# Kernel optimization log

Hardware: AMD Instinct MI355X
Metric: run time of the kernel (lower is better)

## Reference

```python
import jax, jax.numpy as jnp
import numpy as np

N_EMBD = 1024
N_HEAD = 16
HEAD_DIM = N_EMBD // N_HEAD


def setup_inputs() -> dict:
    key = jax.random.key(0)
    k1, k2, k3 = jax.random.split(key, 3)
    x = jax.random.normal(k1, (2, 2048, N_EMBD), dtype=jnp.float32)
    # torch Linear weight shapes: c_attn [3*n_embd, n_embd], c_proj [n_embd, n_embd]
    w_attn = jax.random.normal(k2, (3 * N_EMBD, N_EMBD), dtype=jnp.float32) * 0.02
    w_proj = jax.random.normal(k3, (N_EMBD, N_EMBD), dtype=jnp.float32) * 0.02
    return {"x": x, "w_attn": w_attn, "w_proj": w_proj}


def reference(x, w_attn, w_proj):
    B, T, C = x.shape
    qkv = x @ w_attn.T  # [B,T,3C]
    q, k, v = jnp.split(qkv, 3, axis=2)
    # [B,T,H,D] -> [B,H,T,D]
    def heads(t):
        return t.reshape(B, T, N_HEAD, HEAD_DIM).transpose(0, 2, 1, 3)
    q, k, v = heads(q), heads(k), heads(v)
    scale = 1.0 / jnp.sqrt(jnp.asarray(HEAD_DIM, dtype=x.dtype))
    att = jnp.einsum('bhqd,bhkd->bhqk', q, k) * scale
    causal = jnp.tril(jnp.ones((T, T), dtype=bool))
    att = jnp.where(causal[None, None], att, jnp.asarray(-jnp.inf, dtype=att.dtype))
    att = jax.nn.softmax(att, axis=-1)
    y = jnp.einsum('bhqk,bhkd->bhqd', att, v)
    y = y.transpose(0, 2, 1, 3).reshape(B, T, C)
    return y @ w_proj.T
```

## Files before the change

### kernel.cpp

```cpp
#include <hip/hip_runtime.h>

#define BSZ 2
#define SEQ 2048
#define NEMBD 1024
#define NHEAD 16
#define HDIM 64
#define BT (BSZ * SEQ)
#define QKV_LD (3 * NEMBD)
#define SCALE_LOG2E 0.1803368665f

typedef unsigned short u16;
typedef __attribute__((ext_vector_type(8))) short short8;
typedef __attribute__((ext_vector_type(4))) float floatx4;
typedef __attribute__((ext_vector_type(4))) unsigned short ushort4v;

#define MFMA16(a, b, c) __builtin_amdgcn_mfma_f32_16x16x32_bf16(a, b, c, 0, 0, 0)

__device__ __forceinline__ void gload_lds16(const void* g, void* l) {
  __builtin_amdgcn_global_load_lds(
      (const __attribute__((address_space(1))) unsigned int*)(g),
      (__attribute__((address_space(3))) unsigned int*)(l), 16, 0, 0);
}

__device__ __forceinline__ u16 f2bf(float f) {
  unsigned int u = __builtin_bit_cast(unsigned int, f);
  u += 0x7FFFu + ((u >> 16) & 1u);
  return (u16)(u >> 16);
}

__device__ __forceinline__ float bf2f(u16 v) {
  return __builtin_bit_cast(float, (unsigned)v << 16);
}

#define N_X  (BT * NEMBD)
#define N_WA (QKV_LD * NEMBD)
#define N_WP (NEMBD * NEMBD)
__global__ __launch_bounds__(256) void cvt_all(const float* __restrict__ x,
                                               const float* __restrict__ wa,
                                               const float* __restrict__ wp,
                                               u16* __restrict__ xb,
                                               u16* __restrict__ wab,
                                               u16* __restrict__ wpb) {
  int i = (blockIdx.x * 256 + threadIdx.x) * 8;
  const float* src;
  u16* dst;
  if (i < N_X)            { src = x + i;              dst = xb + i; }
  else if (i < N_X + N_WA){ src = wa + (i - N_X);     dst = wab + (i - N_X); }
  else                    { src = wp + (i - N_X - N_WA); dst = wpb + (i - N_X - N_WA); }
  float4 a = *(const float4*)(src);
  float4 b = *(const float4*)(src + 4);
  short8 o;
  o[0] = (short)f2bf(a.x); o[1] = (short)f2bf(a.y);
  o[2] = (short)f2bf(a.z); o[3] = (short)f2bf(a.w);
  o[4] = (short)f2bf(b.x); o[5] = (short)f2bf(b.y);
  o[6] = (short)f2bf(b.z); o[7] = (short)f2bf(b.w);
  *(short8*)(dst) = o;
}

__global__ __launch_bounds__(256) void gemm_qkv(const u16* __restrict__ A,
                                                const u16* __restrict__ B,
                                                u16* __restrict__ qkb,
                                                u16* __restrict__ vtg) {
  __shared__ __align__(16) u16 As[128 * 64];
  __shared__ __align__(16) u16 Bs[128 * 64];
  const int t = threadIdx.x;
  const int lane = t & 63, w = t >> 6;
  const int l15 = lane & 15, quad = lane >> 4;
  const int wm = w >> 1, wn = w & 1;
  const int m0 = blockIdx.y * 128, n0 = blockIdx.x * 128;
  const int is_v = (n0 >= 2 * NEMBD);

  floatx4 acc[4][4] = {};

  for (int k0 = 0; k0 < NEMBD; k0 += 64) {
    __syncthreads();
#pragma unroll
    for (int is = 0; is < 4; ++is) {
      int s = is * 256 + t;
      int row = s >> 3, pos = s & 7;
      int kc = pos ^ (row & 7);
      gload_lds16(A + (size_t)(m0 + row) * NEMBD + k0 + kc * 8, &As[s * 8]);
      gload_lds16(B + (size_t)(n0 + row) * NEMBD + k0 + kc * 8, &Bs[s * 8]);
    }
    __syncthreads();
#pragma unroll
    for (int kh = 0; kh < 2; ++kh) {
      short8 af[4], bfr[4];
#pragma unroll
      for (int mt = 0; mt < 4; ++mt) {
        int row = wm * 64 + mt * 16 + l15;
        af[mt] = *(const short8*)&As[row * 64 + (((kh * 4 + quad) ^ (row & 7)) * 8)];
      }
#pragma unroll
      for (int nt = 0; nt < 4; ++nt) {
        int row = wn * 64 + nt * 16 + l15;
        bfr[nt] = *(const short8*)&Bs[row * 64 + (((kh * 4 + quad) ^ (row & 7)) * 8)];
      }
      if (is_v) {
#pragma unroll
        for (int mt = 0; mt < 4; ++mt)
#pragma unroll
          for (int nt = 0; nt < 4; ++nt)
            acc[mt][nt] = MFMA16(af[mt], bfr[nt], acc[mt][nt]);
      } else {
#pragma unroll
        for (int mt = 0; mt < 4; ++mt)
#pragma unroll
          for (int nt = 0; nt < 4; ++nt)
            acc[mt][nt] = MFMA16(bfr[nt], af[mt], acc[mt][nt]);
      }
    }
  }

  if (is_v) {
#pragma unroll
    for (int mt = 0; mt < 4; ++mt)
#pragma unroll
      for (int nt = 0; nt < 4; ++nt) {
        int hd = n0 + wn * 64 + nt * 16 + l15 - 2 * NEMBD;
        int token = m0 + wm * 64 + mt * 16 + quad * 4;
        int b = token >> 11, tp = token & (SEQ - 1);
        ushort4v pk;
#pragma unroll
        for (int r = 0; r < 4; ++r) pk[r] = f2bf(acc[mt][nt][r]);
        *(ushort4v*)&vtg[((size_t)(b * NEMBD + hd)) * SEQ + tp] = pk;
      }
  } else {
#pragma unroll
    for (int mt = 0; mt < 4; ++mt) {
      size_t token = (size_t)(m0 + wm * 64 + mt * 16 + l15);
#pragma unroll
      for (int nt = 0; nt < 4; ++nt) {
        int nc = n0 + wn * 64 + nt * 16 + quad * 4;
        ushort4v pk;
#pragma unroll
        for (int r = 0; r < 4; ++r) pk[r] = f2bf(acc[mt][nt][r]);
        *(ushort4v*)&qkb[token * 2048 + nc] = pk;
      }
    }
  }
}

__global__ __launch_bounds__(256) void attn_mfma4(const u16* __restrict__ qkb,
                                                  const u16* __restrict__ vtg,
                                                  u16* __restrict__ opart,
                                                  float* __restrict__ lpart) {
  const int bx = blockIdx.x;
  const int qt = 15 - (bx >> 6);
  const int r6 = bx & 63;
  const int bh = r6 >> 1, half = r6 & 1;
  const int b = bh >> 4, h = bh & 15;
  const int t = threadIdx.x, lane = t & 63, w = t >> 6;
  const int l15 = lane & 15, quad = lane >> 4;

  __shared__ __align__(16) u16 S[25600];
  u16* Qs  = S;
  u16* KV0 = S + 8192;
  u16* KV1 = S;
  u16* Pa  = S + 16384;

  const int kt0 = half ? (qt + 1) : 0;
  const int nkt = qt + 1;

  {
    const u16* qb = qkb + ((size_t)(b * SEQ + qt * 128)) * 2048 + h * HDIM;
#pragma unroll
    for (int is = 0; is < 4; ++is) {
      int s = is * 256 + t;
      int row = s >> 3, pos = s & 7;
      int kc = pos ^ (row & 7);
      gload_lds16(qb + (size_t)row * 2048 + kc * 8, &Qs[s * 8]);
    }
  }

#define STAGE_KV(KT, BUF)                                                      \
  {                                                                            \
    const u16* kb_ = qkb + ((size_t)(b * SEQ + (KT) * 64)) * 2048 + NEMBD + h * HDIM; \
    const u16* vb_ = vtg + ((size_t)(bh * 64)) * SEQ + (KT) * 64;              \
    _Pragma("unroll")                                                          \
    for (int is = 0; is < 2; ++is) {                                           \
      int s = is * 256 + t;                                                    \
      int row = s >> 3, pos = s & 7;                                           \
      int kc = pos ^ (row & 7);                                                \
      gload_lds16(kb_ + (size_t)row * 2048 + kc * 8, &(BUF)[s * 8]);           \
      gload_lds16(vb_ + (size_t)row * SEQ + kc * 8, &(BUF)[4096 + s * 8]);     \
    }                                                                          \
  }

  STAGE_KV(kt0, KV0);
  __syncthreads();

  short8 qf[2][2];
#pragma unroll
  for (int qs = 0; qs < 2; ++qs) {
    int qrow = w * 32 + qs * 16 + l15;
#pragma unroll
    for (int hf = 0; hf < 2; ++hf)
      qf[qs][hf] = *(const short8*)&Qs[qrow * 64 + (((hf * 4 + quad) ^ (qrow & 7)) * 8)];
  }
  __syncthreads();

  float rs[2] = {0.f, 0.f};
  floatx4 o_acc[2][4] = {};

#define COMPUTE_TILE(BUF, KT, MASKED)                                          \
  {                                                                            \
    floatx4 sacc[2][4];                                                        \
    _Pragma("unroll")                                                          \
    for (int nt = 0; nt < 4; ++nt) {                                           \
      int krow = nt * 16 + l15;                                                \
      short8 kf0 = *(const short8*)&(BUF)[krow * 64 + ((quad ^ (krow & 7)) * 8)]; \
      short8 kf1 = *(const short8*)&(BUF)[krow * 64 + (((4 + quad) ^ (krow & 7)) * 8)]; \
      _Pragma("unroll")                                                        \
      for (int qs = 0; qs < 2; ++qs) {                                         \
        floatx4 z = {0.f, 0.f, 0.f, 0.f};                                      \
        z = MFMA16(kf0, qf[qs][0], z);                                         \
        z = MFMA16(kf1, qf[qs][1], z);                                         \
        sacc[qs][nt] = z;                                                      \
      }                                                                        \
    }                                                                          \
    _Pragma("unroll")                                                          \
    for (int qs = 0; qs < 2; ++qs) {                                           \
      const int qg = qt * 128 + w * 32 + qs * 16 + l15;                        \
      const int kb0 = (KT) * 64 + quad * 4;                                    \
      _Pragma("unroll")                                                        \
      for (int nt = 0; nt < 4; ++nt) {                                         \
        ushort4v pk;                                                           \
        _Pragma("unroll")                                                      \
        for (int r = 0; r < 4; ++r) {                                          \
          float p = exp2f(fmaf(sacc[qs][nt][r], SCALE_LOG2E, -8.0f));          \
          if (MASKED && (kb0 + nt * 16 + r) > qg) p = 0.0f;                    \
          rs[qs] += p;                                                         \
          pk[r] = f2bf(p);                                                     \
        }                                                                      \
        *(ushort4v*)&Pa[(w * 32 + qs * 16 + l15) * 72 + nt * 16 + quad * 4] = pk; \
      }                                                                        \
    }                                                                          \
    short8 pf[2][2];                                                           \
    _Pragma("unroll")                                                          \
    for (int qs = 0; qs < 2; ++qs) {                                           \
      const int prow = w * 32 + qs * 16 + l15;                                 \
      pf[qs][0] = *(const short8*)&Pa[prow * 72 + quad * 8];                   \
      pf[qs][1] = *(const short8*)&Pa[prow * 72 + 32 + quad * 8];              \
    }                                                                          \
    _Pragma("unroll")                                                          \
    for (int nt = 0; nt < 4; ++nt) {                                           \
      int drow = nt * 16 + l15;                                                \
      short8 vf0 = *(const short8*)&(BUF)[4096 + drow * 64 + ((quad ^ (drow & 7)) * 8)]; \
      short8 vf1 = *(const short8*)&(BUF)[4096 + drow * 64 + (((4 + quad) ^ (drow & 7)) * 8)]; \
      _Pragma("unroll")                                                        \
      for (int qs = 0; qs < 2; ++qs) {                                         \
        o_acc[qs][nt] = MFMA16(pf[qs][0], vf0, o_acc[qs][nt]);                 \
        o_acc[qs][nt] = MFMA16(pf[qs][1], vf1, o_acc[qs][nt]);                 \
      }                                                                        \
    }                                                                          \
  }

  for (int i = 0; i < nkt; ++i) {
    const int kt = kt0 + i;
    u16* cur = (i & 1) ? KV1 : KV0;
    u16* nxt = (i & 1) ? KV0 : KV1;
    if (i + 1 < nkt) STAGE_KV(kt0 + i + 1, nxt);
    if (kt >= 2 * qt) { COMPUTE_TILE(cur, kt, 1); }
    else              { COMPUTE_TILE(cur, kt, 0); }
    __syncthreads();
  }
#undef COMPUTE_TILE
#undef STAGE_KV

#pragma unroll
  for (int qs = 0; qs < 2; ++qs) {
    rs[qs] += __shfl_xor(rs[qs], 16, 64);
    rs[qs] += __shfl_xor(rs[qs], 32, 64);
    if (quad == 0)
      lpart[((size_t)half * 32 + bh) * SEQ + qt * 128 + w * 32 + qs * 16 + l15] = rs[qs];
  }
  u16* ob = opart + (size_t)half * BT * NEMBD;
#pragma unroll
  for (int qs = 0; qs < 2; ++qs)
#pragma unroll
    for (int nt = 0; nt < 4; ++nt)
#pragma unroll
      for (int r = 0; r < 4; ++r) {
        size_t tok = (size_t)(b * SEQ + qt * 128 + w * 32 + qs * 16 + quad * 4 + r);
        ob[tok * NEMBD + h * HDIM + nt * 16 + l15] = f2bf(o_acc[qs][nt][r]);
      }
}

__global__ __launch_bounds__(256) void combine(const u16* __restrict__ opart,
                                               const float* __restrict__ lpart,
                                               u16* __restrict__ yb) {
  int idx = (blockIdx.x * 256 + threadIdx.x) * 4;
  int tok = idx >> 10, c = idx & 1023;
  int b = tok >> 11, q = tok & (SEQ - 1), h = c >> 6;
  float l = lpart[(size_t)(b * 16 + h) * SEQ + q] +
            lpart[(size_t)(32 + b * 16 + h) * SEQ + q];
  float inv = 1.0f / l;
  ushort4v o0 = *(const ushort4v*)&opart[idx];
  ushort4v o1 = *(const ushort4v*)&opart[(size_t)BT * NEMBD + idx];
  ushort4v yo;
#pragma unroll
  for (int j = 0; j < 4; ++j) {
    float f0 = bf2f(o0[j]);
    float f1 = bf2f(o1[j]);
    yo[j] = f2bf((f0 + f1) * inv);
  }
  *(ushort4v*)&yb[idx] = yo;
}

__global__ __launch_bounds__(256) void gemm_out(const u16* __restrict__ A,
                                                const u16* __restrict__ B,
                                                float* __restrict__ C) {
  __shared__ __align__(16) u16 As[128 * 64];
  __shared__ __align__(16) u16 Bs[64 * 64];
  const int t = threadIdx.x;
  const int lane = t & 63, w = t >> 6;
  const int l15 = lane & 15, quad = lane >> 4;
  const int wm = w >> 1, wn = w & 1;
  const int m0 = blockIdx.y * 128, n0 = blockIdx.x * 64;

  floatx4 acc[4][2] = {};

  for (int k0 = 0; k0 < NEMBD; k0 += 64) {
    __syncthreads();
#pragma unroll
    for (int is = 0; is < 4; ++is) {
      int s = is * 256 + t;
      int row = s >> 3, pos = s & 7;
      int kc = pos ^ (row & 7);
      gload_lds16(A + (size_t)(m0 + row) * NEMBD + k0 + kc * 8, &As[s * 8]);
    }
#pragma unroll
    for (int is = 0; is < 2; ++is) {
      int s = is * 256 + t;
      int row = s >> 3, pos = s & 7;
      int kc = pos ^ (row & 7);
      gload_lds16(B + (size_t)(n0 + row) * NEMBD + k0 + kc * 8, &Bs[s * 8]);
    }
    __syncthreads();
#pragma unroll
    for (int kh = 0; kh < 2; ++kh) {
      short8 af[4], bfr[2];
#pragma unroll
      for (int mt = 0; mt < 4; ++mt) {
        int row = wm * 64 + mt * 16 + l15;
        af[mt] = *(const short8*)&As[row * 64 + (((kh * 4 + quad) ^ (row & 7)) * 8)];
      }
#pragma unroll
      for (int nt = 0; nt < 2; ++nt) {
        int row = wn * 32 + nt * 16 + l15;
        bfr[nt] = *(const short8*)&Bs[row * 64 + (((kh * 4 + quad) ^ (row & 7)) * 8)];
      }
#pragma unroll
      for (int mt = 0; mt < 4; ++mt)
#pragma unroll
        for (int nt = 0; nt < 2; ++nt)
          acc[mt][nt] = MFMA16(bfr[nt], af[mt], acc[mt][nt]);
    }
  }

#pragma unroll
  for (int mt = 0; mt < 4; ++mt) {
    size_t token = (size_t)(m0 + wm * 64 + mt * 16 + l15);
#pragma unroll
    for (int nt = 0; nt < 2; ++nt) {
      int nc = n0 + wn * 32 + nt * 16 + quad * 4;
      float4 v = make_float4(acc[mt][nt][0], acc[mt][nt][1],
                             acc[mt][nt][2], acc[mt][nt][3]);
      *(float4*)&C[token * NEMBD + nc] = v;
    }
  }
}

extern "C" void kernel_launch(void* const* d_in, const int* in_sizes, int n_in,
                              void* d_out, int out_size, void* d_ws, size_t ws_size,
                              hipStream_t stream) {
  const float* x      = (const float*)d_in[0];
  const float* w_attn = (const float*)d_in[1];
  const float* w_proj = (const float*)d_in[2];
  float* out = (float*)d_out;

  u16* base  = (u16*)d_ws;
  u16* opart = base;
  u16* xb    = base;
  u16* wab   = base + 4194304;
  u16* wpb   = base + 8388608;
  u16* qkb   = base + 9437184;
  u16* vtg   = base + 17825792;
  u16* yb    = base + 22020096;
  float* lpart = (float*)(base + 26214400);

  cvt_all<<<(N_X + N_WA + N_WP) / 2048, 256, 0, stream>>>(x, w_attn, w_proj, xb, wab, wpb);

  gemm_qkv<<<dim3(QKV_LD / 128, BT / 128), 256, 0, stream>>>(xb, wab, qkb, vtg);

  attn_mfma4<<<dim3((SEQ / 128) * BSZ * NHEAD * 2), 256, 0, stream>>>(qkb, vtg, opart, lpart);

  combine<<<(BT * NEMBD) / 1024, 256, 0, stream>>>(opart, lpart, yb);

  gemm_out<<<dim3(NEMBD / 64, BT / 128), 256, 0, stream>>>(yb, wpb, out);
}
```

Before: 199.2 us.

## Software-pipeline QKV and output projection GEMM k-loops with prefetch

The QKV GEMM now prefetches the next k-tile from global memory into registers while computing on the current LDS tile, then writes those registers to LDS after a barrier. The output-projection GEMM gets double-buffered LDS, issuing direct global-to-LDS loads for the next tile before computing on the current one. Both changes aim to hide global-load latency behind MFMA work. The costs are higher register pressure in the QKV kernel and twice the LDS use in the output kernel, which may lower occupancy.

```diff
diff --git a/kernel.cpp b/kernel.cpp
--- a/kernel.cpp
+++ b/kernel.cpp
@@ -70,19 +70,34 @@
   const int m0 = blockIdx.y * 128, n0 = blockIdx.x * 128;
   const int is_v = (n0 >= 2 * NEMBD);
 
+  const int srow8 = t >> 3;
+  const int kc = (t & 7) ^ (srow8 & 7);
+  const u16* gA = A + (size_t)(m0 + srow8) * NEMBD + kc * 8;
+  const u16* gB = B + (size_t)(n0 + srow8) * NEMBD + kc * 8;
+
   floatx4 acc[4][4] = {};
+  short8 ra[4], rb[4];
+
+#define QKV_LOAD(K0)                                                           \
+  { _Pragma("unroll")                                                          \
+    for (int is = 0; is < 4; ++is) {                                           \
+      ra[is] = *(const short8*)(gA + (size_t)(is * 32) * NEMBD + (K0));        \
+      rb[is] = *(const short8*)(gB + (size_t)(is * 32) * NEMBD + (K0));        \
+    } }
+#define QKV_WRITE()                                                            \
+  { _Pragma("unroll")                                                          \
+    for (int is = 0; is < 4; ++is) {                                           \
+      *(short8*)&As[(is * 256 + t) * 8] = ra[is];                              \
+      *(short8*)&Bs[(is * 256 + t) * 8] = rb[is];                              \
+    } }
+
+  QKV_LOAD(0);
+  QKV_WRITE();
+  __syncthreads();
 
   for (int k0 = 0; k0 < NEMBD; k0 += 64) {
-    __syncthreads();
-#pragma unroll
-    for (int is = 0; is < 4; ++is) {
-      int s = is * 256 + t;
-      int row = s >> 3, pos = s & 7;
-      int kc = pos ^ (row & 7);
-      gload_lds16(A + (size_t)(m0 + row) * NEMBD + k0 + kc * 8, &As[s * 8]);
-      gload_lds16(B + (size_t)(n0 + row) * NEMBD + k0 + kc * 8, &Bs[s * 8]);
-    }
-    __syncthreads();
+    const int more = (k0 + 64 < NEMBD);
+    if (more) QKV_LOAD(k0 + 64);
 #pragma unroll
     for (int kh = 0; kh < 2; ++kh) {
       short8 af[4], bfr[4];
@@ -110,7 +125,14 @@
             acc[mt][nt] = MFMA16(bfr[nt], af[mt], acc[mt][nt]);
       }
     }
-  }
+    __syncthreads();
+    if (more) {
+      QKV_WRITE();
+      __syncthreads();
+    }
+  }
+#undef QKV_LOAD
+#undef QKV_WRITE
 
   if (is_v) {
 #pragma unroll
@@ -311,45 +333,49 @@
 __global__ __launch_bounds__(256) void gemm_out(const u16* __restrict__ A,
                                                 const u16* __restrict__ B,
                                                 float* __restrict__ C) {
-  __shared__ __align__(16) u16 As[128 * 64];
-  __shared__ __align__(16) u16 Bs[64 * 64];
+  __shared__ __align__(16) u16 S[2][12288];
   const int t = threadIdx.x;
   const int lane = t & 63, w = t >> 6;
   const int l15 = lane & 15, quad = lane >> 4;
   const int wm = w >> 1, wn = w & 1;
   const int m0 = blockIdx.y * 128, n0 = blockIdx.x * 64;
 
+  const int srow8 = t >> 3;
+  const int kc = (t & 7) ^ (srow8 & 7);
+
+#define OUT_STAGE(K0, BUF)                                                     \
+  { u16* as_ = &S[BUF][0]; u16* bs_ = &S[BUF][8192];                           \
+    _Pragma("unroll")                                                          \
+    for (int is = 0; is < 4; ++is)                                             \
+      gload_lds16(A + (size_t)(m0 + is * 32 + srow8) * NEMBD + (K0) + kc * 8,  \
+                  &as_[(is * 256 + t) * 8]);                                   \
+    _Pragma("unroll")                                                          \
+    for (int is = 0; is < 2; ++is)                                             \
+      gload_lds16(B + (size_t)(n0 + is * 32 + srow8) * NEMBD + (K0) + kc * 8,  \
+                  &bs_[(is * 256 + t) * 8]); }
+
   floatx4 acc[4][2] = {};
 
-  for (int k0 = 0; k0 < NEMBD; k0 += 64) {
-    __syncthreads();
-#pragma unroll
-    for (int is = 0; is < 4; ++is) {
-      int s = is * 256 + t;
-      int row = s >> 3, pos = s & 7;
-      int kc = pos ^ (row & 7);
-      gload_lds16(A + (size_t)(m0 + row) * NEMBD + k0 + kc * 8, &As[s * 8]);
-    }
-#pragma unroll
-    for (int is = 0; is < 2; ++is) {
-      int s = is * 256 + t;
-      int row = s >> 3, pos = s & 7;
-      int kc = pos ^ (row & 7);
-      gload_lds16(B + (size_t)(n0 + row) * NEMBD + k0 + kc * 8, &Bs[s * 8]);
-    }
-    __syncthreads();
+  OUT_STAGE(0, 0);
+  __syncthreads();
+
+  int ib = 0;
+  for (int k0 = 0; k0 < NEMBD; k0 += 64, ib ^= 1) {
+    if (k0 + 64 < NEMBD) OUT_STAGE(k0 + 64, ib ^ 1);
+    const u16* as_ = &S[ib][0];
+    const u16* bs_ = &S[ib][8192];
 #pragma unroll
     for (int kh = 0; kh < 2; ++kh) {
       short8 af[4], bfr[2];
 #pragma unroll
       for (int mt = 0; mt < 4; ++mt) {
         int row = wm * 64 + mt * 16 + l15;
-        af[mt] = *(const short8*)&As[row * 64 + (((kh * 4 + quad) ^ (row & 7)) * 8)];
+        af[mt] = *(const short8*)&as_[row * 64 + (((kh * 4 + quad) ^ (row & 7)) * 8)];
       }
 #pragma unroll
       for (int nt = 0; nt < 2; ++nt) {
         int row = wn * 32 + nt * 16 + l15;
-        bfr[nt] = *(const short8*)&Bs[row * 64 + (((kh * 4 + quad) ^ (row & 7)) * 8)];
+        bfr[nt] = *(const short8*)&bs_[row * 64 + (((kh * 4 + quad) ^ (row & 7)) * 8)];
       }
 #pragma unroll
       for (int mt = 0; mt < 4; ++mt)
@@ -357,7 +383,9 @@
         for (int nt = 0; nt < 2; ++nt)
           acc[mt][nt] = MFMA16(bfr[nt], af[mt], acc[mt][nt]);
     }
-  }
+    __syncthreads();
+  }
+#undef OUT_STAGE
 
 #pragma unroll
   for (int mt = 0; mt < 4; ++mt) {
```

Result: faster. 187.6 us (-5.8%).
